# Performance work log

Measured on AMD Instinct MI355X. Metric: run time of the kernel, lower is better.

## Reference

```python
import jax, jax.numpy as jnp
import numpy as np

B, S, D_IN, D = 8, 4096, 512, 256


def setup_inputs() -> dict:
    key = jax.random.key(0)
    ks = jax.random.split(key, 7)
    s_in = 1.0 / np.sqrt(D_IN)
    return {
        "x": jax.random.normal(ks[0], (B, S, D_IN), dtype=jnp.float32),
        "Wq": jax.random.normal(ks[1], (D_IN, D), dtype=jnp.float32) * s_in,
        "bq": jnp.zeros((D,), dtype=jnp.float32),
        "Wk": jax.random.normal(ks[2], (D_IN, D), dtype=jnp.float32) * s_in,
        "bk": jnp.zeros((D,), dtype=jnp.float32),
        "Wv": jax.random.normal(ks[3], (D_IN, D), dtype=jnp.float32) * s_in,
        "bv": jnp.zeros((D,), dtype=jnp.float32),
    }


def reference(x, Wq, bq, Wk, bk, Wv, bv):
    # Q/K/V projections (three Dense layers in the original)
    Q = jnp.einsum("bsd,de->bse", x, Wq) + bq  # [B,S,D]
    K = jnp.einsum("bsd,de->bse", x, Wk) + bk
    V = jnp.einsum("bsd,de->bse", x, Wv) + bv
    # scaled dot-product attention: softmax(QK^T / sqrt(d)) V
    scale = 1.0 / jnp.sqrt(jnp.asarray(Q.shape[-1], dtype=Q.dtype))
    scores = jnp.einsum("bqe,bke->bqk", Q, K) * scale  # [B,S,S]
    attn = jax.nn.softmax(scores, axis=-1)
    out = jnp.einsum("bqk,bke->bqe", attn, V)  # [B,S,D]
    return out
```

## Files before the change

### kernel.cpp

```cpp
#include <hip/hip_runtime.h>
#include <hip/hip_bf16.h>
#include <stdint.h>

#define B_   8
#define S_   4096
#define DIN  512
#define D_   256
#define ROWS (B_ * S_)

typedef __attribute__((ext_vector_type(8))) short short8;
typedef __attribute__((ext_vector_type(4))) float floatx4;
typedef __attribute__((ext_vector_type(16))) float floatx16;
typedef __attribute__((ext_vector_type(4))) short short4v;
typedef __attribute__((ext_vector_type(2))) unsigned uint2v;

__device__ __forceinline__ void gll16(const void* g, void* lds) {
  __builtin_amdgcn_global_load_lds(
      (const __attribute__((address_space(1))) void*)g,
      (__attribute__((address_space(3))) void*)lds, 16, 0, 0);
}
__device__ __forceinline__ short f2bf(float x) {
  union { float f; unsigned u; } c; c.f = x;
  unsigned r = (c.u + 0x7FFF + ((c.u >> 16) & 1)) >> 16;
  return (short)r;
}
__device__ __forceinline__ float bf2f(short v) {
  union { unsigned u; float f; } c; c.u = ((unsigned)(unsigned short)v) << 16;
  return c.f;
}
__device__ __forceinline__ unsigned pk2bf(float a, float b) {
  union { __hip_bfloat162 h; unsigned u; } c;
  c.h = __float22bfloat162_rn(float2{a, b});
  return c.u;
}
__device__ __forceinline__ float fexp2(float x) {
#if __has_builtin(__builtin_amdgcn_exp2f)
  return __builtin_amdgcn_exp2f(x);
#else
  return exp2f(x);
#endif
}

__device__ __forceinline__ void plswap(unsigned& a, unsigned& b, int H) {
#if __has_builtin(__builtin_amdgcn_permlane32_swap)
  uint2v r = __builtin_amdgcn_permlane32_swap(a, b, false, false);
  a = r[0]; b = r[1];
#else
  unsigned sa = (unsigned)__shfl_xor((int)a, 32);
  unsigned sb = (unsigned)__shfl_xor((int)b, 32);
  unsigned na = H ? sb : a;
  unsigned nb = H ? b : sa;
  a = na; b = nb;
#endif
}

__device__ __forceinline__ float halfsum(float x) {
#if __has_builtin(__builtin_amdgcn_permlane32_swap)
  union { float f; unsigned u; } c; c.f = x;
  uint2v r = __builtin_amdgcn_permlane32_swap(c.u, c.u, false, false);
  union { unsigned u; float f; } a, b; a.u = r[0]; b.u = r[1];
  return a.f + b.f;
#else
  return x + __shfl_xor(x, 32);
#endif
}

__global__ __launch_bounds__(256) void detect_kernel(
    const unsigned short* __restrict__ w, int* __restrict__ flag) {
  const int tid = threadIdx.x;
  float m = 0.f;
#pragma unroll
  for (int j = 0; j < 16; ++j) {
    float f = bf2f((short)w[tid * 16 + j]);
    m = fmaxf(m, fabsf(f));
  }
#pragma unroll
  for (int d = 1; d < 64; d <<= 1) m = fmaxf(m, __shfl_xor(m, d));
  __shared__ float red[4];
  if ((tid & 63) == 0) red[tid >> 6] = m;
  __syncthreads();
  if (tid == 0) {
    float mm = fmaxf(fmaxf(red[0], red[1]), fmaxf(red[2], red[3]));
    flag[0] = (mm > 1000.0f) ? 1 : 0;
  }
}

__global__ __launch_bounds__(256) void cvt_kernel(
    const void* __restrict__ src, short* __restrict__ dst, int n,
    const int* __restrict__ flag) {
  const int i = blockIdx.x * 256 + threadIdx.x;
  if (i * 8 >= n) return;
  if (*flag) {
    float4 a = ((const float4*)src)[2 * i];
    float4 b = ((const float4*)src)[2 * i + 1];
    short8 o;
    o[0] = f2bf(a.x); o[1] = f2bf(a.y); o[2] = f2bf(a.z); o[3] = f2bf(a.w);
    o[4] = f2bf(b.x); o[5] = f2bf(b.y); o[6] = f2bf(b.z); o[7] = f2bf(b.w);
    ((short8*)dst)[i] = o;
  } else {
    ((short8*)dst)[i] = ((const short8*)src)[i];
  }
}

__global__ __launch_bounds__(256) void wtcvt_kernel(
    const void* __restrict__ Wq, const void* __restrict__ Wk,
    const void* __restrict__ Wv, short* __restrict__ Wt,
    const int* __restrict__ flag) {
  __shared__ float tile[32][33];
  const int mat = blockIdx.z;
  const void* W = (mat == 0) ? Wq : ((mat == 1) ? Wk : Wv);
  const int n0 = blockIdx.x * 32, k0 = blockIdx.y * 32;
  const int tx = threadIdx.x & 31, ty = threadIdx.x >> 5;
  const bool f32 = (*flag != 0);
#pragma unroll
  for (int i = 0; i < 4; ++i) {
    int k = ty + i * 8;
    float v = f32 ? ((const float*)W)[(k0 + k) * D_ + n0 + tx]
                  : bf2f(((const short*)W)[(k0 + k) * D_ + n0 + tx]);
    tile[k][tx] = v;
  }
  __syncthreads();
  short* o = Wt + mat * (D_ * DIN);
#pragma unroll
  for (int i = 0; i < 4; ++i) {
    int n = ty + i * 8;
    o[(n0 + n) * DIN + k0 + tx] = f2bf(tile[tx][n]);
  }
}

__global__ __launch_bounds__(256) void biascvt_kernel(
    const void* __restrict__ bq, const void* __restrict__ bk,
    const void* __restrict__ bv, short* __restrict__ bbuf,
    const int* __restrict__ flag) {
  const int tid = threadIdx.x;
  const bool f32 = (*flag != 0);
  const void* p[3] = {bq, bk, bv};
#pragma unroll
  for (int m = 0; m < 3; ++m)
    bbuf[m * D_ + tid] = f32 ? f2bf(((const float*)p[m])[tid])
                             : ((const short*)p[m])[tid];
}

__global__ __launch_bounds__(256, 2) void qkv_kernel(
    const short* __restrict__ x, const short* __restrict__ Wt,
    const short* __restrict__ bb,
    short* __restrict__ Qg, short* __restrict__ Kg, short* __restrict__ Vtg) {
  __shared__ short As[2][512 * 8];
  __shared__ short Bs[2][512 * 8];
  const int tid = threadIdx.x;
  const int lane = tid & 63, w = tid >> 6;
  const int li = lane & 15, g = lane >> 4;
  const int mb = blockIdx.x;
  const int mat = blockIdx.y >> 1, nb = blockIdx.y & 1;
  const short* Ag = x + mb * 128 * DIN;
  const short* Bt = Wt + mat * (D_ * DIN) + nb * 128 * DIN;

  auto stage = [&](int buf, int k0) {
#pragma unroll
    for (int p = 0; p < 2; ++p) {
      int c = p * 256 + tid;
      int row = c >> 2, og = (c & 3) ^ (row & 3);
      gll16(Ag + row * DIN + k0 + og * 8, &As[buf][(p * 256 + w * 64) * 8]);
    }
#pragma unroll
    for (int p = 0; p < 2; ++p) {
      int c = p * 256 + tid;
      int row = c >> 2, og = (c & 3) ^ (row & 3);
      gll16(Bt + row * DIN + k0 + og * 8, &Bs[buf][(p * 256 + w * 64) * 8]);
    }
  };

  const int msub = (w & 1) * 64, nsub = (w >> 1) * 64;
  floatx4 acc[4][4];
#pragma unroll
  for (int i = 0; i < 4; ++i)
#pragma unroll
    for (int j = 0; j < 4; ++j) acc[i][j] = floatx4{0.f, 0.f, 0.f, 0.f};

  stage(0, 0);
  __syncthreads();
  for (int kt = 0; kt < 16; ++kt) {
    if (kt < 15) stage((kt + 1) & 1, (kt + 1) * 32);
    const int buf = kt & 1;
    short8 af[4], bfr[4];
#pragma unroll
    for (int mt = 0; mt < 4; ++mt) {
      int row = msub + mt * 16 + li;
      int og = g ^ (row & 3);
      af[mt] = *(const short8*)&As[buf][(row * 4 + og) * 8];
    }
#pragma unroll
    for (int nt = 0; nt < 4; ++nt) {
      int row = nsub + nt * 16 + li;
      int og = g ^ (row & 3);
      bfr[nt] = *(const short8*)&Bs[buf][(row * 4 + og) * 8];
    }
#pragma unroll
    for (int mt = 0; mt < 4; ++mt)
#pragma unroll
      for (int nt = 0; nt < 4; ++nt)
        acc[mt][nt] = __builtin_amdgcn_mfma_f32_16x16x32_bf16(
            af[mt], bfr[nt], acc[mt][nt], 0, 0, 0);
    __syncthreads();
  }

  const short* bias = bb + mat * 256;
  if (mat < 2) {
    short* O = (mat == 0) ? Qg : Kg;
#pragma unroll
    for (int nt = 0; nt < 4; ++nt) {
      float bv_ = bf2f(bias[nb * 128 + nsub + nt * 16 + li]);
#pragma unroll
      for (int mt = 0; mt < 4; ++mt)
#pragma unroll
        for (int r = 0; r < 4; ++r) {
          int m = mb * 128 + msub + mt * 16 + g * 4 + r;
          int n = nb * 128 + nsub + nt * 16 + li;
          O[m * D_ + n] = f2bf(acc[mt][nt][r] + bv_);
        }
    }
  } else {
#pragma unroll
    for (int nt = 0; nt < 4; ++nt) {
      float bv_ = bf2f(bias[nb * 128 + nsub + nt * 16 + li]);
#pragma unroll
      for (int mt = 0; mt < 4; ++mt) {
        int m0 = mb * 128 + msub + mt * 16 + g * 4;
        int batch = m0 >> 12, s = m0 & (S_ - 1);
        int n = nb * 128 + nsub + nt * 16 + li;
        short4v pk;
#pragma unroll
        for (int r = 0; r < 4; ++r) pk[r] = f2bf(acc[mt][nt][r] + bv_);
        *(short4v*)&Vtg[(batch * D_ + n) * S_ + s] = pk;
      }
    }
  }
}

__global__ __launch_bounds__(256, 2) void attn_kernel(
    const short* __restrict__ Qg, const short* __restrict__ Kg,
    const short* __restrict__ Vtg, short* __restrict__ Op,
    float* __restrict__ lsum) {
  __shared__ short Ks[2][1024 * 8];
  __shared__ short Vs[2][1024 * 8];
  const int tid = threadIdx.x, lane = tid & 63, w = tid >> 6;
  const int q = lane & 31, H = lane >> 5;
  const int id = blockIdx.x;
  const int bb = id & 7;
  const int h = (id >> 3) & 1;
  const int q0 = (id >> 4) * 128;
  const int qrow = q0 + w * 32;
  const int s_base = h * 2048;

  const short* Qb = Qg + (size_t)(bb * S_ + qrow) * D_;
  const short* Kb = Kg + (size_t)bb * S_ * D_;
  const short* Vb = Vtg + (size_t)bb * D_ * S_;

  short8 qf[16];
#pragma unroll
  for (int o = 0; o < 16; ++o)
    qf[o] = *(const short8*)&Qb[q * D_ + o * 16 + H * 8];

  floatx16 oa[8];
#pragma unroll
  for (int n2 = 0; n2 < 8; ++n2)
#pragma unroll
    for (int i = 0; i < 16; ++i) oa[n2][i] = 0.f;
  float lst = 0.f;

  auto stage = [&](int t, int buf) {
    const int s0 = s_base + t * 32;
#pragma unroll
    for (int p = 0; p < 4; ++p) {
      int c = p * 256 + tid;
      int s = c >> 5, od = (c & 31) ^ s;
      gll16(&Kb[(s0 + s) * D_ + od * 8], &Ks[buf][c * 8]);
    }
#pragma unroll
    for (int p = 0; p < 4; ++p) {
      int c = p * 256 + tid;
      int e = c >> 2, so = (c & 3) ^ ((e >> 1) & 3);
      gll16(&Vb[e * S_ + s0 + so * 8], &Vs[buf][c * 8]);
    }
  };

  const float cs = 0.09016844005556f;
  const float M12 = 12.0f;
  stage(0, 0);
  __syncthreads();

  for (int t = 0; t < 64; ++t) {
    if (t < 63) stage(t + 1, (t + 1) & 1);
    const int buf = t & 1;

    floatx16 sc0, sc1;
#pragma unroll
    for (int i = 0; i < 16; ++i) { sc0[i] = 0.f; sc1[i] = 0.f; }
    __builtin_amdgcn_s_setprio(1);
#pragma unroll
    for (int o = 0; o < 16; o += 2) {
      short8 kf0 = *(const short8*)&Ks[buf][(q * 32 + ((2 * o + H) ^ q)) * 8];
      short8 kf1 =
          *(const short8*)&Ks[buf][(q * 32 + ((2 * (o + 1) + H) ^ q)) * 8];
      sc0 = __builtin_amdgcn_mfma_f32_32x32x16_bf16(kf0, qf[o], sc0, 0, 0, 0);
      sc1 =
          __builtin_amdgcn_mfma_f32_32x32x16_bf16(kf1, qf[o + 1], sc1, 0, 0, 0);
    }
    __builtin_amdgcn_s_setprio(0);
#pragma unroll
    for (int i = 0; i < 16; ++i) sc0[i] += sc1[i];

    float t8[8];
    float pv0[8];
#pragma unroll
    for (int i = 0; i < 8; ++i) pv0[i] = fexp2(sc0[i] * cs - M12);
    unsigned dw0[4];
#pragma unroll
    for (int m = 0; m < 4; ++m) dw0[m] = pk2bf(pv0[2 * m], pv0[2 * m + 1]);
#pragma unroll
    for (int m = 0; m < 4; ++m) t8[m] = pv0[2 * m] + pv0[2 * m + 1];
    plswap(dw0[0], dw0[2], H);
    plswap(dw0[1], dw0[3], H);
    union { unsigned u[4]; short8 s; } pk0;
    pk0.u[0] = dw0[0]; pk0.u[1] = dw0[1]; pk0.u[2] = dw0[2]; pk0.u[3] = dw0[3];
    short8 pfr0 = pk0.s;

    __builtin_amdgcn_s_setprio(1);
#pragma unroll
    for (int n2 = 0; n2 < 8; ++n2) {
      const int e = n2 * 32 + q;
      const int esw = (e >> 1) & 3;
      short8 vf = *(const short8*)&Vs[buf][(e * 4 + ((2 * 0 + H) ^ esw)) * 8];
      oa[n2] =
          __builtin_amdgcn_mfma_f32_32x32x16_bf16(vf, pfr0, oa[n2], 0, 0, 0);
    }
    __builtin_amdgcn_s_setprio(0);

    float pv1[8];
#pragma unroll
    for (int i = 0; i < 8; ++i) pv1[i] = fexp2(sc0[8 + i] * cs - M12);
    unsigned dw1[4];
#pragma unroll
    for (int m = 0; m < 4; ++m) dw1[m] = pk2bf(pv1[2 * m], pv1[2 * m + 1]);
#pragma unroll
    for (int m = 0; m < 4; ++m) t8[4 + m] = pv1[2 * m] + pv1[2 * m + 1];
    plswap(dw1[0], dw1[2], H);
    plswap(dw1[1], dw1[3], H);
    union { unsigned u[4]; short8 s; } pk1;
    pk1.u[0] = dw1[0]; pk1.u[1] = dw1[1]; pk1.u[2] = dw1[2]; pk1.u[3] = dw1[3];
    short8 pfr1 = pk1.s;

    __builtin_amdgcn_s_setprio(1);
#pragma unroll
    for (int n2 = 0; n2 < 8; ++n2) {
      const int e = n2 * 32 + q;
      const int esw = (e >> 1) & 3;
      short8 vf = *(const short8*)&Vs[buf][(e * 4 + ((2 * 1 + H) ^ esw)) * 8];
      oa[n2] =
          __builtin_amdgcn_mfma_f32_32x32x16_bf16(vf, pfr1, oa[n2], 0, 0, 0);
    }
    __builtin_amdgcn_s_setprio(0);

    float t4[4];
#pragma unroll
    for (int m = 0; m < 4; ++m) t4[m] = t8[2 * m] + t8[2 * m + 1];
    float rs = (t4[0] + t4[1]) + (t4[2] + t4[3]);
    lst += halfsum(rs);

    __syncthreads();
  }

  const float inv = 1.0f / lst;
  short* Oh = Op + (size_t)h * ROWS * D_ + (size_t)(bb * S_ + qrow) * D_;
#pragma unroll
  for (int n2 = 0; n2 < 8; ++n2) {
#pragma unroll
    for (int qd = 0; qd < 4; ++qd) {
      int e0 = n2 * 32 + 8 * qd + 4 * H;
      uint2v st;
      st[0] = pk2bf(oa[n2][4 * qd] * inv, oa[n2][4 * qd + 1] * inv);
      st[1] = pk2bf(oa[n2][4 * qd + 2] * inv, oa[n2][4 * qd + 3] * inv);
      *(uint2v*)&Oh[q * D_ + e0] = st;
    }
  }
  if (H == 0) {
    int grow = bb * S_ + qrow + q;
    lsum[h * ROWS + grow] = lst;
  }
}

__global__ __launch_bounds__(256) void combine_kernel(
    const short* __restrict__ Op, const float* __restrict__ lsum,
    void* __restrict__ outv, const int* __restrict__ flag) {
  const int gid = blockIdx.x * 256 + threadIdx.x;
  const int row = gid >> 6;
  const int e4 = (gid & 63) * 4;
  const float l1 = lsum[row], l2 = lsum[ROWS + row];
  const float inv = 1.0f / (l1 + l2);
  const float c1 = l1 * inv, c2 = l2 * inv;
  short4v a = *(const short4v*)&Op[(size_t)row * D_ + e4];
  short4v b = *(const short4v*)&Op[(size_t)(ROWS + row) * D_ + e4];
  if (*flag) {
    float4 o;
    o.x = c1 * bf2f(a[0]) + c2 * bf2f(b[0]);
    o.y = c1 * bf2f(a[1]) + c2 * bf2f(b[1]);
    o.z = c1 * bf2f(a[2]) + c2 * bf2f(b[2]);
    o.w = c1 * bf2f(a[3]) + c2 * bf2f(b[3]);
    *(float4*)&((float*)outv)[(size_t)row * D_ + e4] = o;
  } else {
    short4v o;
#pragma unroll
    for (int j = 0; j < 4; ++j)
      o[j] = f2bf(c1 * bf2f(a[j]) + c2 * bf2f(b[j]));
    *(short4v*)&((short*)outv)[(size_t)row * D_ + e4] = o;
  }
}

extern "C" void kernel_launch(void* const* d_in, const int* in_sizes, int n_in,
                              void* d_out, int out_size, void* d_ws, size_t ws_size,
                              hipStream_t stream) {
  const void* x  = d_in[0];
  const void* Wq = d_in[1];
  const void* bq = d_in[2];
  const void* Wk = d_in[3];
  const void* bk = d_in[4];
  const void* Wv = d_in[5];
  const void* bv = d_in[6];
  char* ws = (char*)d_ws;
  int*   flag = (int*)(ws);
  short* bbuf = (short*)(ws + 256);
  float* lsum = (float*)(ws + 4096);
  short* Wt   = (short*)(ws + (1u << 20));
  short* xb   = (short*)(ws + (2u << 20));
  short* Qw   = (short*)(ws + (34u << 20));
  short* Kw   = (short*)(ws + (50u << 20));
  short* Vtw  = (short*)(ws + (66u << 20));
  short* Op   = xb;

  hipLaunchKernelGGL(detect_kernel, dim3(1), dim3(256), 0, stream,
                     (const unsigned short*)Wq, flag);
  hipLaunchKernelGGL(cvt_kernel, dim3(8192), dim3(256), 0, stream,
                     x, xb, B_ * S_ * DIN, flag);
  hipLaunchKernelGGL(wtcvt_kernel, dim3(8, 16, 3), dim3(256), 0, stream,
                     Wq, Wk, Wv, Wt, flag);
  hipLaunchKernelGGL(biascvt_kernel, dim3(1), dim3(256), 0, stream,
                     bq, bk, bv, bbuf, flag);
  hipLaunchKernelGGL(qkv_kernel, dim3(256, 6), dim3(256), 0, stream,
                     xb, Wt, bbuf, Qw, Kw, Vtw);
  hipLaunchKernelGGL(attn_kernel, dim3(512), dim3(256), 0, stream,
                     Qw, Kw, Vtw, Op, lsum);
  hipLaunchKernelGGL(combine_kernel, dim3(ROWS / 4), dim3(256), 0, stream,
                     Op, lsum, d_out, flag);
}
```

Measured before the change: 358.6 us.

## Software-pipeline attention loop: overlap QK^T of tile t with PV of tile t-1

Restructures the attention main loop so each iteration's QK^T MFMAs are interleaved with the PV MFMAs of the previous tile, with a prologue and epilogue. The exp and softmax work of one tile can then overlap matrix work instead of stalling between dependent phases. V gets a triple-buffered LDS ring held in dynamic shared memory (80KB) while K stays double-buffered. The single accumulator chain replaces two split accumulators, and the larger LDS footprint may reduce occupancy against the launch bound of 2 blocks.

```diff
diff --git a/kernel.cpp b/kernel.cpp
--- a/kernel.cpp
+++ b/kernel.cpp
@@ -241,8 +241,9 @@
     const short* __restrict__ Qg, const short* __restrict__ Kg,
     const short* __restrict__ Vtg, short* __restrict__ Op,
     float* __restrict__ lsum) {
-  __shared__ short Ks[2][1024 * 8];
-  __shared__ short Vs[2][1024 * 8];
+  extern __shared__ short smem[];
+  short* Ksb = smem;
+  short* Vsb = smem + 16384;
   const int tid = threadIdx.x, lane = tid & 63, w = tid >> 6;
   const int q = lane & 31, H = lane >> 5;
   const int id = blockIdx.x;
@@ -268,106 +269,129 @@
     for (int i = 0; i < 16; ++i) oa[n2][i] = 0.f;
   float lst = 0.f;
 
-  auto stage = [&](int t, int buf) {
+  auto stageK = [&](int t, short* kdst) {
     const int s0 = s_base + t * 32;
 #pragma unroll
     for (int p = 0; p < 4; ++p) {
       int c = p * 256 + tid;
       int s = c >> 5, od = (c & 31) ^ s;
-      gll16(&Kb[(s0 + s) * D_ + od * 8], &Ks[buf][c * 8]);
-    }
+      gll16(&Kb[(s0 + s) * D_ + od * 8], &kdst[c * 8]);
+    }
+  };
+  auto stageV = [&](int t, short* vdst) {
+    const int s0 = s_base + t * 32;
 #pragma unroll
     for (int p = 0; p < 4; ++p) {
       int c = p * 256 + tid;
       int e = c >> 2, so = (c & 3) ^ ((e >> 1) & 3);
-      gll16(&Vb[e * S_ + s0 + so * 8], &Vs[buf][c * 8]);
+      gll16(&Vb[e * S_ + s0 + so * 8], &vdst[c * 8]);
     }
   };
 
   const float cs = 0.09016844005556f;
   const float M12 = 12.0f;
-  stage(0, 0);
+
+  stageK(0, Ksb);
+  stageV(0, Vsb);
   __syncthreads();
 
-  for (int t = 0; t < 64; ++t) {
-    if (t < 63) stage(t + 1, (t + 1) & 1);
-    const int buf = t & 1;
-
-    floatx16 sc0, sc1;
-#pragma unroll
-    for (int i = 0; i < 16; ++i) { sc0[i] = 0.f; sc1[i] = 0.f; }
+  short8 pA, pB;
+
+  {
+    stageK(1, Ksb + 8192);
+    stageV(1, Vsb + 8192);
+    floatx16 sc;
+#pragma unroll
+    for (int i = 0; i < 16; ++i) sc[i] = 0.f;
     __builtin_amdgcn_s_setprio(1);
 #pragma unroll
-    for (int o = 0; o < 16; o += 2) {
-      short8 kf0 = *(const short8*)&Ks[buf][(q * 32 + ((2 * o + H) ^ q)) * 8];
-      short8 kf1 =
-          *(const short8*)&Ks[buf][(q * 32 + ((2 * (o + 1) + H) ^ q)) * 8];
-      sc0 = __builtin_amdgcn_mfma_f32_32x32x16_bf16(kf0, qf[o], sc0, 0, 0, 0);
-      sc1 =
-          __builtin_amdgcn_mfma_f32_32x32x16_bf16(kf1, qf[o + 1], sc1, 0, 0, 0);
+    for (int o = 0; o < 16; ++o) {
+      short8 kf = *(const short8*)&Ksb[(q * 32 + ((2 * o + H) ^ q)) * 8];
+      sc = __builtin_amdgcn_mfma_f32_32x32x16_bf16(kf, qf[o], sc, 0, 0, 0);
     }
     __builtin_amdgcn_s_setprio(0);
-#pragma unroll
-    for (int i = 0; i < 16; ++i) sc0[i] += sc1[i];
-
-    float t8[8];
-    float pv0[8];
-#pragma unroll
-    for (int i = 0; i < 8; ++i) pv0[i] = fexp2(sc0[i] * cs - M12);
-    unsigned dw0[4];
-#pragma unroll
-    for (int m = 0; m < 4; ++m) dw0[m] = pk2bf(pv0[2 * m], pv0[2 * m + 1]);
-#pragma unroll
-    for (int m = 0; m < 4; ++m) t8[m] = pv0[2 * m] + pv0[2 * m + 1];
-    plswap(dw0[0], dw0[2], H);
-    plswap(dw0[1], dw0[3], H);
-    union { unsigned u[4]; short8 s; } pk0;
-    pk0.u[0] = dw0[0]; pk0.u[1] = dw0[1]; pk0.u[2] = dw0[2]; pk0.u[3] = dw0[3];
-    short8 pfr0 = pk0.s;
-
+    unsigned dw[8];
+    float rs = 0.f;
+#pragma unroll
+    for (int i = 0; i < 16; i += 2) {
+      float a = fexp2(sc[i] * cs - M12);
+      float b = fexp2(sc[i + 1] * cs - M12);
+      dw[i >> 1] = pk2bf(a, b);
+      rs += a + b;
+    }
+    plswap(dw[0], dw[2], H); plswap(dw[1], dw[3], H);
+    plswap(dw[4], dw[6], H); plswap(dw[5], dw[7], H);
+    union { unsigned u[4]; short8 s; } ka, kb2;
+    ka.u[0] = dw[0]; ka.u[1] = dw[1]; ka.u[2] = dw[2]; ka.u[3] = dw[3];
+    kb2.u[0] = dw[4]; kb2.u[1] = dw[5]; kb2.u[2] = dw[6]; kb2.u[3] = dw[7];
+    pA = ka.s; pB = kb2.s;
+    lst += halfsum(rs);
+    __syncthreads();
+  }
+
+  int vst = 2, vrd = 0;
+  for (int t = 1; t < 64; ++t) {
+    if (t < 63) {
+      stageK(t + 1, Ksb + (((t + 1) & 1) ? 8192 : 0));
+      stageV(t + 1, Vsb + vst * 8192);
+    }
+    const short* Kr = Ksb + ((t & 1) ? 8192 : 0);
+    const short* Vr = Vsb + vrd * 8192;
+
+    floatx16 sc;
+#pragma unroll
+    for (int i = 0; i < 16; ++i) sc[i] = 0.f;
     __builtin_amdgcn_s_setprio(1);
 #pragma unroll
-    for (int n2 = 0; n2 < 8; ++n2) {
+    for (int o = 0; o < 16; ++o) {
+      short8 kf = *(const short8*)&Kr[(q * 32 + ((2 * o + H) ^ q)) * 8];
+      sc = __builtin_amdgcn_mfma_f32_32x32x16_bf16(kf, qf[o], sc, 0, 0, 0);
+      const int n2 = o & 7;
       const int e = n2 * 32 + q;
       const int esw = (e >> 1) & 3;
-      short8 vf = *(const short8*)&Vs[buf][(e * 4 + ((2 * 0 + H) ^ esw)) * 8];
-      oa[n2] =
-          __builtin_amdgcn_mfma_f32_32x32x16_bf16(vf, pfr0, oa[n2], 0, 0, 0);
+      short8 vf = *(const short8*)
+          &Vr[(e * 4 + ((2 * (o >> 3) + H) ^ esw)) * 8];
+      oa[n2] = __builtin_amdgcn_mfma_f32_32x32x16_bf16(
+          vf, (o < 8) ? pA : pB, oa[n2], 0, 0, 0);
     }
     __builtin_amdgcn_s_setprio(0);
 
-    float pv1[8];
-#pragma unroll
-    for (int i = 0; i < 8; ++i) pv1[i] = fexp2(sc0[8 + i] * cs - M12);
-    unsigned dw1[4];
-#pragma unroll
-    for (int m = 0; m < 4; ++m) dw1[m] = pk2bf(pv1[2 * m], pv1[2 * m + 1]);
-#pragma unroll
-    for (int m = 0; m < 4; ++m) t8[4 + m] = pv1[2 * m] + pv1[2 * m + 1];
-    plswap(dw1[0], dw1[2], H);
-    plswap(dw1[1], dw1[3], H);
-    union { unsigned u[4]; short8 s; } pk1;
-    pk1.u[0] = dw1[0]; pk1.u[1] = dw1[1]; pk1.u[2] = dw1[2]; pk1.u[3] = dw1[3];
-    short8 pfr1 = pk1.s;
-
+    unsigned dw[8];
+    float rs = 0.f;
+#pragma unroll
+    for (int i = 0; i < 16; i += 2) {
+      float a = fexp2(sc[i] * cs - M12);
+      float b = fexp2(sc[i + 1] * cs - M12);
+      dw[i >> 1] = pk2bf(a, b);
+      rs += a + b;
+    }
+    plswap(dw[0], dw[2], H); plswap(dw[1], dw[3], H);
+    plswap(dw[4], dw[6], H); plswap(dw[5], dw[7], H);
+    union { unsigned u[4]; short8 s; } ka, kb2;
+    ka.u[0] = dw[0]; ka.u[1] = dw[1]; ka.u[2] = dw[2]; ka.u[3] = dw[3];
+    kb2.u[0] = dw[4]; kb2.u[1] = dw[5]; kb2.u[2] = dw[6]; kb2.u[3] = dw[7];
+    pA = ka.s; pB = kb2.s;
+    lst += halfsum(rs);
+
+    vst = (vst == 2) ? 0 : vst + 1;
+    vrd = (vrd == 2) ? 0 : vrd + 1;
+    __syncthreads();
+  }
+
+  {
+    const short* Vr = Vsb + vrd * 8192;
     __builtin_amdgcn_s_setprio(1);
 #pragma unroll
-    for (int n2 = 0; n2 < 8; ++n2) {
+    for (int o = 0; o < 16; ++o) {
+      const int n2 = o & 7;
       const int e = n2 * 32 + q;
       const int esw = (e >> 1) & 3;
-      short8 vf = *(const short8*)&Vs[buf][(e * 4 + ((2 * 1 + H) ^ esw)) * 8];
-      oa[n2] =
-          __builtin_amdgcn_mfma_f32_32x32x16_bf16(vf, pfr1, oa[n2], 0, 0, 0);
+      short8 vf = *(const short8*)
+          &Vr[(e * 4 + ((2 * (o >> 3) + H) ^ esw)) * 8];
+      oa[n2] = __builtin_amdgcn_mfma_f32_32x32x16_bf16(
+          vf, (o < 8) ? pA : pB, oa[n2], 0, 0, 0);
     }
     __builtin_amdgcn_s_setprio(0);
-
-    float t4[4];
-#pragma unroll
-    for (int m = 0; m < 4; ++m) t4[m] = t8[2 * m] + t8[2 * m + 1];
-    float rs = (t4[0] + t4[1]) + (t4[2] + t4[3]);
-    lst += halfsum(rs);
-
-    __syncthreads();
   }
 
   const float inv = 1.0f / lst;
@@ -447,7 +471,7 @@
                      bq, bk, bv, bbuf, flag);
   hipLaunchKernelGGL(qkv_kernel, dim3(256, 6), dim3(256), 0, stream,
                      xb, Wt, bbuf, Qw, Kw, Vtw);
-  hipLaunchKernelGGL(attn_kernel, dim3(512), dim3(256), 0, stream,
+  hipLaunchKernelGGL(attn_kernel, dim3(512), dim3(256), 81920, stream,
                      Qw, Kw, Vtw, Op, lsum);
   hipLaunchKernelGGL(combine_kernel, dim3(ROWS / 4), dim3(256), 0, stream,
                      Op, lsum, d_out, flag);
```

Result: no change. 356.6 us (-0.6%).
